# Kernel optimization log

Measured on AMD Instinct MI355X. Metric: run time of the kernel, lower is better.

The kernel has to match this reference:

```python
import jax, jax.numpy as jnp
import numpy as np

B, T, N, DIN = 32, 12, 512, 1
H, K, ED, HOR, OD = 64, 3, 10, 12, 1


def setup_inputs() -> dict:
    key = jax.random.key(0)
    ks = jax.random.split(key, 15)
    rn = lambda k, s, sc=0.1: jax.random.normal(k, s, jnp.float32) * sc
    return {
        "source": jax.random.normal(ks[0], (B, T, N, DIN), jnp.float32),
        "targets": jax.random.normal(ks[1], (B, HOR, N, OD), jnp.float32),
        # standard Gumbel(0,1) noise: -log(Exp(1)), matches torch's exponential_().log()
        "gumbel_noise": -jnp.log(jax.random.exponential(ks[2], (N, N, 2), jnp.float32)),
        "emb": jax.random.normal(ks[3], (N, ED), jnp.float32),
        "gw0": rn(ks[4], (ED, K, DIN + H, 2 * H)),
        "gb0": rn(ks[5], (ED, 2 * H)),
        "uw0": rn(ks[6], (ED, K, DIN + H, H)),
        "ub0": rn(ks[7], (ED, H)),
        "gw1": rn(ks[8], (ED, K, 2 * H, 2 * H)),
        "gb1": rn(ks[9], (ED, 2 * H)),
        "uw1": rn(ks[10], (ED, K, 2 * H, H)),
        "ub1": rn(ks[11], (ED, H)),
        "cw": rn(ks[12], (HOR * OD, 1, 1, H)),  # Conv2d(1, HOR*OD, (1, H)) weight
        "cb": rn(ks[13], (HOR * OD,)),
    }


def scaled_laplacian(emb, gnoise):
    sim = emb @ emb.T                                   # [N,N]
    nrm = jnp.linalg.norm(emb, axis=1, keepdims=True)
    lg = sim / (nrm @ nrm.T)
    lg = (lg + 1.0) / 2.0
    logits = jnp.stack([lg, 1.0 - lg], axis=-1)         # [N,N,2]
    # faithful to the pasted gumbel_softmax: y_soft = gumbels (no softmax), tau=1, hard=True
    y_soft = logits + gnoise
    idx = jnp.argmax(y_soft, axis=-1)
    y_hard = jax.nn.one_hot(idx, 2, dtype=logits.dtype)
    ret = y_hard - jax.lax.stop_gradient(y_soft) + y_soft
    adj = ret[:, :, 0] * (1.0 - jnp.eye(N, dtype=logits.dtype))  # zero diagonal
    d = jnp.sum(adj, axis=1)
    L = -adj + jnp.diag(d)                              # diag(adj)=0, so L diag = d
    lam = jnp.max(L) - jnp.min(L)
    tilde = 2.0 * L / lam - jnp.eye(N, dtype=logits.dtype)
    return tilde


def cheb_supports(tilde):
    sup = [jnp.eye(N, dtype=tilde.dtype), tilde]
    for _ in range(2, K):
        sup.append(2.0 * tilde @ sup[-1] - sup[-2])
    return jnp.stack(sup, axis=0)                       # [K,N,N]


def gconv(x, emb, supports, wp, bp):
    # x: [B,N,C]; wp: [ED,K,C,O]; bp: [ED,O]
    xg = jnp.einsum('knm,bmc->bnkc', supports, x)
    w = jnp.einsum('nd,dkio->nkio', emb, wp)
    b = emb @ bp                                        # [N,O]
    return jnp.einsum('bnki,nkio->bno', xg, w) + b


def run_layer(inputs, emb, supports, gw, gb, uw, ub):
    # inputs: [B,T,N,C] -> hidden states [B,T,N,H]
    h0 = jnp.zeros((inputs.shape[0], N, H), inputs.dtype)

    def step(h, x_t):
        xs = jnp.concatenate([x_t, h], axis=-1)
        zr = jax.nn.sigmoid(gconv(xs, emb, supports, gw, gb))
        z, r = zr[..., :H], zr[..., H:]
        cand = jnp.concatenate([x_t, z * h], axis=-1)
        hc = jnp.tanh(gconv(cand, emb, supports, uw, ub))
        h_new = r * h + (1.0 - r) * hc
        return h_new, h_new

    _, hs = jax.lax.scan(step, h0, jnp.swapaxes(inputs, 0, 1))
    return jnp.swapaxes(hs, 0, 1)


def reference(source, targets, gumbel_noise, emb, gw0, gb0, uw0, ub0,
              gw1, gb1, uw1, ub1, cw, cb):
    tilde = scaled_laplacian(emb, gumbel_noise)
    supports = cheb_supports(tilde)
    h1 = run_layer(source, emb, supports, gw0, gb0, uw0, ub0)
    h2 = run_layer(h1, emb, supports, gw1, gb1, uw1, ub1)
    last = h2[:, -1, :, :]                              # [B,N,H]
    # Conv2d(1, HOR*OD, (1,H)) over [B,1,N,H] == per-node linear
    y = jnp.einsum('bnh,oh->bon', last, cw[:, 0, 0, :]) + cb[None, :, None]
    y = y.reshape(-1, HOR, OD, N)
    return jnp.transpose(y, (0, 1, 3, 2))               # [B,HOR,N,OD]
```

## Files before the change

kernel.cpp:

```cpp
#include <hip/hip_runtime.h>
#include <math.h>

#define N_    512
#define B_    32
#define T_    12
#define H_    64
#define ED_   10
#define HOR_  12
#define OUTS_ 4096

typedef unsigned short ushort_t;
typedef __attribute__((ext_vector_type(4))) float f32x4;
typedef __attribute__((ext_vector_type(8))) __bf16 bf16x8;
typedef __attribute__((ext_vector_type(8))) short short8;

__device__ __forceinline__ float sigmoidf_(float x){ return 1.f/(1.f+expf(-x)); }
__device__ __forceinline__ float b2f(ushort_t u){ return __uint_as_float(((unsigned)u)<<16); }
__device__ __forceinline__ ushort_t f2b(float f){
  unsigned x = __float_as_uint(f);
  unsigned r = x + 0x7FFFu + ((x>>16)&1u);
  return (ushort_t)(r>>16);
}
__device__ __forceinline__ void stage16(const void* g, void* l){
  __builtin_amdgcn_global_load_lds(
    (const __attribute__((address_space(1))) unsigned int*)g,
    (__attribute__((address_space(3))) unsigned int*)l, 16, 0, 0);
}

__global__ __launch_bounds__(512) void k_norm(const float* __restrict__ emb, float* __restrict__ nrm){
  int n = threadIdx.x;
  if (n < N_){
    float s = 0.f;
    #pragma unroll
    for (int d=0; d<ED_; ++d){ float v = emb[n*ED_+d]; s += v*v; }
    nrm[n] = sqrtf(s);
  }
}

__global__ __launch_bounds__(256) void k_adj(const float* __restrict__ emb, const float* __restrict__ nrm,
                      const float* __restrict__ gn, ushort_t* __restrict__ Abf, float* __restrict__ dvec){
  __shared__ float ei[ED_];
  __shared__ float red[256];
  int i = blockIdx.x;
  if (threadIdx.x < ED_) ei[threadIdx.x] = emb[i*ED_+threadIdx.x];
  __syncthreads();
  float ni = nrm[i];
  float part = 0.f;
  for (int j = threadIdx.x; j < N_; j += 256){
    float dot = 0.f;
    #pragma unroll
    for (int d=0; d<ED_; ++d) dot += ei[d]*emb[j*ED_+d];
    float lg = (dot/(ni*nrm[j]) + 1.f)*0.5f;
    size_t gi = ((size_t)i*N_ + j)*2;
    float y0 = lg + gn[gi];
    float y1 = (1.f - lg) + gn[gi+1];
    bool a = (j != i && y0 >= y1);
    Abf[(size_t)i*N_ + j] = a ? (ushort_t)0x3F80 : (ushort_t)0;
    part += a ? 1.f : 0.f;
  }
  red[threadIdx.x] = part;
  __syncthreads();
  for (int s=128; s>0; s>>=1){
    if (threadIdx.x < s) red[threadIdx.x] += red[threadIdx.x+s];
    __syncthreads();
  }
  if (threadIdx.x==0) dvec[i] = red[0];
}

__global__ __launch_bounds__(512) void k_lam(const float* __restrict__ dvec, float* __restrict__ lam){
  __shared__ float red[512];
  red[threadIdx.x] = dvec[threadIdx.x];
  __syncthreads();
  for (int s=256; s>0; s>>=1){
    if (threadIdx.x < s) red[threadIdx.x] = fmaxf(red[threadIdx.x], red[threadIdx.x+s]);
    __syncthreads();
  }
  if (threadIdx.x==0){
    float maxd = red[0];
    lam[0] = maxd + (maxd > 0.f ? 1.f : 0.f);
  }
}

__global__ __launch_bounds__(256) void k_a2(const ushort_t* __restrict__ Abf, ushort_t* __restrict__ A2bf){
  __shared__ float ar[N_];
  int n = blockIdx.x;
  for (int p = threadIdx.x; p < N_; p += 256) ar[p] = b2f(Abf[(size_t)n*N_ + p]);
  __syncthreads();
  int m0 = threadIdx.x, m1 = threadIdx.x + 256;
  float a0 = 0.f, a1 = 0.f;
  for (int p=0; p<N_; ++p){
    float ap = ar[p];
    a0 += ap * b2f(Abf[(size_t)p*N_ + m0]);
    a1 += ap * b2f(Abf[(size_t)p*N_ + m1]);
  }
  A2bf[(size_t)n*N_ + m0] = f2b(a0);
  A2bf[(size_t)n*N_ + m1] = f2b(a1);
}

__global__ __launch_bounds__(256) void k_admats(const ushort_t* __restrict__ Abf, const float* __restrict__ dvec,
                        const float* __restrict__ lam, ushort_t* __restrict__ ADh){
  int idx = blockIdx.x*256 + threadIdx.x;
  int m = idx & (N_-1);
  float dm = 2.f*dvec[m]/lam[0] - 1.f;
  ADh[idx] = Abf[idx] ? f2b(dm) : (ushort_t)0;
}

#define XTILE_USH 8192
__global__ __launch_bounds__(256) void k_apply(
    const ushort_t* __restrict__ XH, const ushort_t* __restrict__ XL,
    const ushort_t* __restrict__ Abf, const ushort_t* __restrict__ A2bf, const ushort_t* __restrict__ ADh,
    float* __restrict__ P, float* __restrict__ Rm, float* __restrict__ Qm)
{
  __shared__ ushort_t lds[2*XTILE_USH + 4096];
  const int z = blockIdx.z;
  const ushort_t* M = (z==0)? Abf : (z==1)? A2bf : ADh;
  float* OUT = (z==0)? P : (z==1)? Rm : Qm;
  const int cBase = blockIdx.x<<7, nBase = blockIdx.y<<6;
  const int tid = threadIdx.x, lane = tid&63, w = tid>>6;
  const int lrow = lane>>3, lslot = lane&7;
  const int srck = lslot ^ (lrow&7);
  const char* g0 = (const char*)XH;
  const char* g1 = (const char*)XL;
  const char* g2 = (const char*)M;
  f32x4 acc[2][4];
  #pragma unroll
  for (int i=0;i<2;++i)
    #pragma unroll
    for (int j=0;j<4;++j) acc[i][j] = f32x4{0.f,0.f,0.f,0.f};
  const int fl = lane&15, kq = lane>>4;

  for (int kk=0; kk<512; kk+=64){
    #pragma unroll
    for (int s=0; s<10; ++s){
      int instId = w + s*4;
      int tile = instId>>4, inst = instId&15;
      const char* g = (tile==0? g0 : (tile==1? g1 : g2));
      int rb = (tile<2? cBase : nBase) + inst*8 + lrow;
      stage16(g + (size_t)rb*(N_*2) + kk*2 + srck*16,
              (char*)lds + tile*16384 + inst*1024);
    }
    __syncthreads();
    #pragma unroll
    for (int kh=0; kh<2; ++kh){
      bf16x8 ah[2], alo[2], bm[4];
      #pragma unroll
      for (int fi=0; fi<2; ++fi){
        int row = (w<<5) + (fi<<4) + fl;
        int off = (row<<6) + (((kq + (kh<<2)) ^ (row&7))<<3);
        ah[fi]  = *(const bf16x8*)&lds[off];
        alo[fi] = *(const bf16x8*)&lds[XTILE_USH + off];
      }
      #pragma unroll
      for (int fj=0; fj<4; ++fj){
        int row = (fj<<4) + fl;
        int off = (row<<6) + (((kq + (kh<<2)) ^ (row&7))<<3);
        bm[fj] = *(const bf16x8*)&lds[2*XTILE_USH + off];
      }
      #pragma unroll
      for (int fi=0; fi<2; ++fi)
        #pragma unroll
        for (int fj=0; fj<4; ++fj){
          acc[fi][fj] = __builtin_amdgcn_mfma_f32_16x16x32_bf16(ah[fi],  bm[fj], acc[fi][fj], 0,0,0);
          acc[fi][fj] = __builtin_amdgcn_mfma_f32_16x16x32_bf16(alo[fi], bm[fj], acc[fi][fj], 0,0,0);
        }
    }
    __syncthreads();
  }
  #pragma unroll
  for (int fi=0; fi<2; ++fi){
    int cg = cBase + (w<<5) + (fi<<4) + (kq<<2);
    #pragma unroll
    for (int fj=0; fj<4; ++fj){
      int ng = nBase + (fj<<4) + fl;
      float4 v = make_float4(acc[fi][fj][0], acc[fi][fj][1], acc[fi][fj][2], acc[fi][fj][3]);
      *(float4*)&OUT[(size_t)ng*OUTS_ + cg] = v;
    }
  }
}

__global__ __launch_bounds__(256) void k_wmax(const float* __restrict__ wp, const float* __restrict__ emb,
                       unsigned int* __restrict__ sb, int KI, int O, int KB){
  __shared__ float es[N_*ED_];
  __shared__ float sm[256];
  for (int e = threadIdx.x; e < N_*ED_; e += 256) es[e] = emb[e];
  __syncthreads();
  int G = 256/O;
  int o = threadIdx.x % O;
  int g = threadIdx.x / O;
  int KIend = min(KI, (int)(blockIdx.x+1)*KB);
  int n0 = blockIdx.y*128;
  size_t KIO = (size_t)KI*O;
  float m = 0.f;
  for (int ki = blockIdx.x*KB + g; ki < KIend; ki += G){
    float wv[ED_];
    #pragma unroll
    for (int d=0; d<ED_; ++d) wv[d] = wp[(size_t)d*KIO + (size_t)ki*O + o];
    for (int n=n0; n<n0+128; ++n){
      float a = 0.f;
      #pragma unroll
      for (int d=0; d<ED_; ++d) a += es[n*ED_+d]*wv[d];
      m = fmaxf(m, fabsf(a));
    }
  }
  sm[threadIdx.x] = m;
  __syncthreads();
  for (int s=128; s>=O; s>>=1){
    if (threadIdx.x < s) sm[threadIdx.x] = fmaxf(sm[threadIdx.x], sm[threadIdx.x+s]);
    __syncthreads();
  }
  if (threadIdx.x < O) atomicMax(&sb[o], __float_as_uint(sm[threadIdx.x]));
}

__global__ __launch_bounds__(256) void k_wquant(const float* __restrict__ wp, const float* __restrict__ emb,
                         const unsigned int* __restrict__ sb, short* __restrict__ W,
                         int KI, int O, int RS){
  __shared__ float es[N_*ED_];
  for (int e = threadIdx.x; e < N_*ED_; e += 256) es[e] = emb[e];
  __syncthreads();
  int KC = RS/8;
  int e = blockIdx.x*256 + threadIdx.x;
  if (e >= KC*O) return;
  int o = e % O, kc = e / O;
  int KIO = KI*O;
  float M = __uint_as_float(sb[o]);
  float inv = (M > 0.f) ? 32767.f/M : 0.f;
  float wv[8][ED_];
  #pragma unroll
  for (int km=0; km<8; ++km){
    int ki = kc*8 + km;
    #pragma unroll
    for (int d=0; d<ED_; ++d)
      wv[km][d] = (ki < KI) ? wp[(size_t)d*KIO + (size_t)ki*O + o] : 0.f;
  }
  int n0 = blockIdx.y*32;
  for (int n=n0; n<n0+32; ++n){
    short8 q;
    #pragma unroll
    for (int km=0; km<8; ++km){
      float a = 0.f;
      #pragma unroll
      for (int d=0; d<ED_; ++d) a += es[n*ED_+d]*wv[km][d];
      q[km] = (short)__float2int_rn(a*inv);
    }
    *(short8*)&W[(((size_t)n*KC + kc)*O + o)*8] = q;
  }
}

__global__ __launch_bounds__(256) void k_bias(const float* __restrict__ bp, const float* __restrict__ emb,
                       float* __restrict__ Bo, int O){
  int idx = blockIdx.x*256 + threadIdx.x;
  int o = idx % O, n = idx / O;
  float a = 0.f;
  #pragma unroll
  for (int d=0; d<ED_; ++d) a += emb[n*ED_+d]*bp[d*O+o];
  Bo[idx] = a;
}

__global__ void k_fill0(float* __restrict__ p, size_t n){
  size_t i = (size_t)blockIdx.x*blockDim.x + threadIdx.x;
  size_t stride = (size_t)gridDim.x*blockDim.x;
  for (; i<n; i+=stride) p[i] = 0.f;
}

__global__ __launch_bounds__(256) void k_btr(const float* __restrict__ S0, const float* __restrict__ S1,
        ushort_t* __restrict__ XH, ushort_t* __restrict__ XL, int CIN, int coff0, int coff1,
        const float* __restrict__ src, int t, int doSrc){
  __shared__ float Tt[64][65];
  const float* S = blockIdx.z ? S1 : S0;
  int coff = blockIdx.z ? coff1 : coff0;
  int mt = blockIdx.x, b = blockIdx.y;
  int r = threadIdx.x >> 6;
  int j = threadIdx.x & 63;
  #pragma unroll
  for (int rr=0; rr<16; ++rr){
    int m = mt*64 + rr*4 + r;
    Tt[rr*4+r][j] = S[((size_t)m*B_ + b)*H_ + j];
  }
  if (doSrc && blockIdx.z==0 && threadIdx.x < 64){
    int m = mt*64 + threadIdx.x;
    float x = src[((size_t)(b*T_+t))*N_ + m];
    size_t o = ((size_t)(b*CIN))*N_ + m;
    ushort_t xh = f2b(x);
    XH[o] = xh; XL[o] = f2b(x - b2f(xh));
  }
  __syncthreads();
  int mr = threadIdx.x & 63;
  int jq = threadIdx.x >> 6;
  #pragma unroll
  for (int jj=0; jj<16; ++jj){
    int jcol = jj*4 + jq;
    float x = Tt[mr][jcol];
    size_t idx = ((size_t)(b*CIN + coff + jcol))*N_ + mt*64 + mr;
    ushort_t xh = f2b(x);
    XH[idx] = xh;
    XL[idx] = f2b(x - b2f(xh));
  }
}

template<int KC, int NBJ, int OSTR, int AS>
__device__ __forceinline__ void contract_i16(const short* __restrict__ Wb,
                                             const float* __restrict__ A0,
                                             float acc[4][NBJ]){
  short8 w0,w1,w2,w3, p0,p1,p2,p3, q0,q1,q2,q3;
  {
    const short8* wp8 = (const short8*)(Wb);
    w0=wp8[0]; w1=wp8[1]; w2=wp8[2]; w3=wp8[3];
    const short8* pp8 = (const short8*)(Wb + OSTR);
    p0=pp8[0]; p1=pp8[1]; p2=pp8[2]; p3=pp8[3];
    q0=p0; q1=p1; q2=p2; q3=p3;
  }
  for (int kc=0; kc<KC; ++kc){
    if (kc+2 < KC){
      const short8* np8 = (const short8*)(Wb + (size_t)(kc+2)*OSTR);
      q0=np8[0]; q1=np8[1]; q2=np8[2]; q3=np8[3];
    }
    #pragma unroll
    for (int kh=0; kh<2; ++kh){
      f32x4 av[NBJ];
      #pragma unroll
      for (int bj=0; bj<NBJ; ++bj) av[bj] = *(const f32x4*)&A0[bj*AS + kc*8 + kh*4];
      #pragma unroll
      for (int u=0; u<4; ++u){
        float f0=(float)w0[kh*4+u], f1=(float)w1[kh*4+u];
        float f2v=(float)w2[kh*4+u], f3=(float)w3[kh*4+u];
        #pragma unroll
        for (int bj=0; bj<NBJ; ++bj){
          acc[0][bj] += av[bj][u]*f0;
          acc[1][bj] += av[bj][u]*f1;
          acc[2][bj] += av[bj][u]*f2v;
          acc[3][bj] += av[bj][u]*f3;
        }
      }
    }
    w0=p0; w1=p1; w2=p2; w3=p3;
    p0=q0; p1=q1; p2=q2; p3=q3;
  }
}

template<int CIN>
__global__ __launch_bounds__(256) void k_gate(
    const float* __restrict__ src, int t,
    const float* __restrict__ hx, const float* __restrict__ hy,
    const float* __restrict__ P, const float* __restrict__ Rm, const float* __restrict__ Qm,
    const float* __restrict__ dvec, const float* __restrict__ lam,
    const short* __restrict__ W, const float* __restrict__ Wsc, const float* __restrict__ Bb,
    const float* __restrict__ hstate,
    float* __restrict__ cand, float* __restrict__ rbuf)
{
  constexpr int O  = 128;
  constexpr int RS = (3*CIN + 7) & ~7;
  constexpr int KC = RS/8;
  constexpr int AS = RS + 4;
  __shared__ float A[B_*AS];
  int n = blockIdx.x;
  float lm = lam[0];
  float al = -2.f/lm;
  float dn = 2.f*dvec[n]/lm - 1.f;
  float c_r = 2.f*al*al, c_q = 2.f*al, c_p = 2.f*al*dn, c_x = 2.f*dn*dn - 1.f;
  for (int e = threadIdx.x; e < B_*CIN; e += 256){
    int b = e/CIN, c = e%CIN;
    float x;
    if (CIN==65) x = (c==0) ? src[((size_t)(b*T_+t))*N_ + n] : hx[(size_t)n*(B_*H_) + b*H_ + (c-1)];
    else         x = (c<H_) ? hx[(size_t)n*(B_*H_) + b*H_ + c] : hy[(size_t)n*(B_*H_) + b*H_ + (c-H_)];
    size_t pi = (size_t)n*OUTS_ + e;
    float pe = P[pi], re = Rm[pi], qe = Qm[pi];
    float* Ab = A + b*AS;
    Ab[c]         = x;
    Ab[CIN+c]     = al*pe + dn*x;
    Ab[2*CIN+c]   = c_r*re + c_q*qe + c_p*pe + c_x*x;
  }
  for (int e = threadIdx.x; e < B_*(AS-3*CIN); e += 256){
    int b = e/(AS-3*CIN), c = e%(AS-3*CIN);
    A[b*AS + 3*CIN + c] = 0.f;
  }
  __syncthreads();
  int ow = threadIdx.x & 31;
  int bq = threadIdx.x >> 5;
  int o0 = ow*4;
  float acc[4][4] = {};
  const short* Wb = W + ((size_t)n*KC*O + o0)*8;
  const float* A0 = A + (bq*4)*AS;
  contract_i16<KC,4,O*8,AS>(Wb, A0, acc);
  #pragma unroll
  for (int oj=0; oj<4; ++oj){
    int o = o0 + oj;
    float sc = Wsc[o]*(1.f/32767.f);
    float bias = Bb[n*O+o];
    if (o < H_){
      #pragma unroll
      for (int bj=0; bj<4; ++bj){
        int b = bq*4 + bj;
        float z = sigmoidf_(acc[oj][bj]*sc + bias);
        size_t hi = (size_t)n*(B_*H_) + b*H_ + o;
        cand[hi] = z*hstate[hi];
      }
    } else {
      int oo = o - H_;
      #pragma unroll
      for (int bj=0; bj<4; ++bj){
        int b = bq*4 + bj;
        rbuf[(size_t)n*(B_*H_) + b*H_ + oo] = sigmoidf_(acc[oj][bj]*sc + bias);
      }
    }
  }
}

template<int CIN>
__global__ __launch_bounds__(256) void k_update(
    const float* __restrict__ src, int t,
    const float* __restrict__ hx, const float* __restrict__ cand,
    const float* __restrict__ P, const float* __restrict__ Rm, const float* __restrict__ Qm,
    const float* __restrict__ dvec, const float* __restrict__ lam,
    const short* __restrict__ W, const float* __restrict__ Wsc, const float* __restrict__ Bb,
    const float* __restrict__ rbuf, float* __restrict__ h)
{
  constexpr int O  = 64;
  constexpr int RS = (3*CIN + 7) & ~7;
  constexpr int KC = RS/8;
  constexpr int AS = RS + 4;
  __shared__ float A[B_*AS];
  int n = blockIdx.x;
  float lm = lam[0];
  float al = -2.f/lm;
  float dn = 2.f*dvec[n]/lm - 1.f;
  float c_r = 2.f*al*al, c_q = 2.f*al, c_p = 2.f*al*dn, c_x = 2.f*dn*dn - 1.f;
  for (int e = threadIdx.x; e < B_*CIN; e += 256){
    int b = e/CIN, c = e%CIN;
    float x;
    if (CIN==65) x = (c==0) ? src[((size_t)(b*T_+t))*N_ + n] : cand[(size_t)n*(B_*H_) + b*H_ + (c-1)];
    else         x = (c<H_) ? hx[(size_t)n*(B_*H_) + b*H_ + c] : cand[(size_t)n*(B_*H_) + b*H_ + (c-H_)];
    size_t pi = (size_t)n*OUTS_ + e;
    float pe = P[pi], re = Rm[pi], qe = Qm[pi];
    float* Ab = A + b*AS;
    Ab[c]         = x;
    Ab[CIN+c]     = al*pe + dn*x;
    Ab[2*CIN+c]   = c_r*re + c_q*qe + c_p*pe + c_x*x;
  }
  for (int e = threadIdx.x; e < B_*(AS-3*CIN); e += 256){
    int b = e/(AS-3*CIN), c = e%(AS-3*CIN);
    A[b*AS + 3*CIN + c] = 0.f;
  }
  __syncthreads();
  int ow = threadIdx.x & 15;
  int bq = threadIdx.x >> 4;
  int o0 = ow*4;
  float acc[4][2] = {};
  const short* Wb = W + ((size_t)n*KC*O + o0)*8;
  const float* A0 = A + (bq*2)*AS;
  contract_i16<KC,2,O*8,AS>(Wb, A0, acc);
  #pragma unroll
  for (int oj=0; oj<4; ++oj){
    int o = o0 + oj;
    float sc = Wsc[o]*(1.f/32767.f);
    float bias = Bb[n*O+o];
    #pragma unroll
    for (int bj=0; bj<2; ++bj){
      int b = bq*2 + bj;
      float hc = tanhf(acc[oj][bj]*sc + bias);
      size_t hidx = (size_t)n*(B_*H_) + b*H_ + o;
      float r = rbuf[hidx];
      h[hidx] = r*h[hidx] + (1.f-r)*hc;
    }
  }
}

__global__ __launch_bounds__(256) void k_readout(const float* __restrict__ hB, const float* __restrict__ cw,
                          const float* __restrict__ cb, float* __restrict__ out){
  int idx = blockIdx.x*256 + threadIdx.x;
  int n = idx & (N_-1);
  int bo = idx >> 9;
  int o = bo % HOR_, b = bo / HOR_;
  float a = cb[o];
  #pragma unroll
  for (int j=0;j<H_;++j) a += hB[(size_t)n*(B_*H_) + b*H_ + j]*cw[o*H_+j];
  out[idx] = a;
}

extern "C" void kernel_launch(void* const* d_in, const int* in_sizes, int n_in,
                              void* d_out, int out_size, void* d_ws, size_t ws_size,
                              hipStream_t stream){
  (void)in_sizes; (void)n_in; (void)out_size; (void)ws_size;
  const float* src  = (const float*)d_in[0];
  const float* gn   = (const float*)d_in[2];
  const float* emb  = (const float*)d_in[3];
  const float* gw0  = (const float*)d_in[4];
  const float* gb0  = (const float*)d_in[5];
  const float* uw0  = (const float*)d_in[6];
  const float* ub0  = (const float*)d_in[7];
  const float* gw1  = (const float*)d_in[8];
  const float* gb1  = (const float*)d_in[9];
  const float* uw1  = (const float*)d_in[10];
  const float* ub1  = (const float*)d_in[11];
  const float* cw   = (const float*)d_in[12];
  const float* cb   = (const float*)d_in[13];
  float* out = (float*)d_out;

  const int RS0 = 200;
  const int RS1 = 384;

  char* ws = (char*)d_ws;
  size_t off = 0;
  auto alloc = [&](size_t bytes)->char*{
    char* p = ws + off; off = (off + bytes + 255) & ~(size_t)255; return p;
  };
  short* Wg0 = (short*)alloc((size_t)N_*128*RS0*2);
  short* Wu0 = (short*)alloc((size_t)N_*64*RS0*2);
  short* Wg1 = (short*)alloc((size_t)N_*128*RS1*2);
  short* Wu1 = (short*)alloc((size_t)N_*64*RS1*2);
  unsigned int* Sg0 = (unsigned int*)alloc(128*4);
  unsigned int* Su0 = (unsigned int*)alloc(64*4);
  unsigned int* Sg1 = (unsigned int*)alloc(128*4);
  unsigned int* Su1 = (unsigned int*)alloc(64*4);
  float* Bg0 = (float*)alloc((size_t)N_*128*4);
  float* Bu0 = (float*)alloc((size_t)N_*64*4);
  float* Bg1 = (float*)alloc((size_t)N_*128*4);
  float* Bu1 = (float*)alloc((size_t)N_*64*4);
  ushort_t* Abf  = (ushort_t*)alloc((size_t)N_*N_*2);
  ushort_t* A2bf = (ushort_t*)alloc((size_t)N_*N_*2);
  ushort_t* ADh  = (ushort_t*)alloc((size_t)N_*N_*2);
  float* dvec = (float*)alloc(N_*4);
  float* lam  = (float*)alloc(256);
  float* nrm  = (float*)alloc(N_*4);
  float* hA   = (float*)alloc((size_t)N_*B_*H_*4);
  float* hB   = (float*)alloc((size_t)N_*B_*H_*4);
  float* rbuf = (float*)alloc((size_t)N_*B_*H_*4);
  float* cand = (float*)alloc((size_t)N_*B_*H_*4);
  ushort_t* XH = (ushort_t*)alloc((size_t)4096*N_*2);
  ushort_t* XL = (ushort_t*)alloc((size_t)4096*N_*2);
  float* P  = (float*)alloc((size_t)N_*OUTS_*4);
  float* R  = (float*)alloc((size_t)N_*OUTS_*4);
  float* Q  = (float*)alloc((size_t)N_*OUTS_*4);

  const float* fSg0 = (const float*)Sg0;
  const float* fSu0 = (const float*)Su0;
  const float* fSg1 = (const float*)Sg1;
  const float* fSu1 = (const float*)Su1;

  k_norm<<<1,512,0,stream>>>(emb, nrm);
  k_adj<<<N_,256,0,stream>>>(emb, nrm, gn, Abf, dvec);
  k_lam<<<1,512,0,stream>>>(dvec, lam);
  k_a2<<<N_,256,0,stream>>>(Abf, A2bf);
  k_admats<<<(N_*N_)/256,256,0,stream>>>(Abf, dvec, lam, ADh);

  k_fill0<<<1,256,0,stream>>>((float*)Sg0, 384);
  k_wmax<<<dim3(17,4),256,0,stream>>>(gw0, emb, Sg0, 195, 128, 12);
  k_wmax<<<dim3(13,4),256,0,stream>>>(uw0, emb, Su0, 195, 64, 16);
  k_wmax<<<dim3(32,4),256,0,stream>>>(gw1, emb, Sg1, 384, 128, 12);
  k_wmax<<<dim3(24,4),256,0,stream>>>(uw1, emb, Su1, 384, 64, 16);
  k_wquant<<<dim3((25*128+255)/256,16),256,0,stream>>>(gw0, emb, Sg0, Wg0, 195, 128, RS0);
  k_wquant<<<dim3((25*64+255)/256,16),256,0,stream>>>(uw0, emb, Su0, Wu0, 195, 64, RS0);
  k_wquant<<<dim3((48*128)/256,16),256,0,stream>>>(gw1, emb, Sg1, Wg1, 384, 128, RS1);
  k_wquant<<<dim3((48*64)/256,16),256,0,stream>>>(uw1, emb, Su1, Wu1, 384, 64, RS1);
  k_bias<<<(N_*128)/256,256,0,stream>>>(gb0, emb, Bg0, 128);
  k_bias<<<(N_*64)/256,256,0,stream>>>(ub0, emb, Bu0, 64);
  k_bias<<<(N_*128)/256,256,0,stream>>>(gb1, emb, Bg1, 128);
  k_bias<<<(N_*64)/256,256,0,stream>>>(ub1, emb, Bu1, 64);

  k_fill0<<<2048,256,0,stream>>>(hA, (size_t)N_*B_*H_);
  k_fill0<<<2048,256,0,stream>>>(hB, (size_t)N_*B_*H_);

  for (int t=0; t<T_; ++t){
    k_btr<<<dim3(8,32,1),256,0,stream>>>(hA, hA, XH, XL, 65, 1, 1, src, t, 1);
    k_apply<<<dim3(17,8,3),256,0,stream>>>(XH, XL, Abf, A2bf, ADh, P, R, Q);
    k_gate<65><<<N_,256,0,stream>>>(src, t, hA, hA, P, R, Q, dvec, lam,
                                    Wg0, fSg0, Bg0, hA, cand, rbuf);
    k_btr<<<dim3(8,32,1),256,0,stream>>>(cand, cand, XH, XL, 65, 1, 1, nullptr, 0, 0);
    k_apply<<<dim3(17,8,3),256,0,stream>>>(XH, XL, Abf, A2bf, ADh, P, R, Q);
    k_update<65><<<N_,256,0,stream>>>(src, t, hA, cand, P, R, Q, dvec, lam,
                                      Wu0, fSu0, Bu0, rbuf, hA);
    k_btr<<<dim3(8,32,2),256,0,stream>>>(hA, hB, XH, XL, 128, 0, 64, nullptr, 0, 0);
    k_apply<<<dim3(32,8,3),256,0,stream>>>(XH, XL, Abf, A2bf, ADh, P, R, Q);
    k_gate<128><<<N_,256,0,stream>>>(nullptr, 0, hA, hB, P, R, Q, dvec, lam,
                                     Wg1, fSg1, Bg1, hB, cand, rbuf);
    k_btr<<<dim3(8,32,1),256,0,stream>>>(cand, cand, XH, XL, 128, 64, 64, nullptr, 0, 0);
    k_apply<<<dim3(32,8,3),256,0,stream>>>(XH, XL, Abf, A2bf, ADh, P, R, Q);
    k_update<128><<<N_,256,0,stream>>>(nullptr, 0, hA, cand, P, R, Q, dvec, lam,
                                       Wu1, fSu1, Bu1, rbuf, hB);
  }

  k_readout<<<(B_*HOR_*N_)/256,256,0,stream>>>(hB, cw, cb, out);
}
```

Before: 2.929 ms.

## Fuse three support-matrix GEMMs into one k_apply pass sharing the X tile

k_apply now computes the products against Abf, A2bf and ADh in a single block. It stages one 64-column X tile (hi and lo halves) plus all three 64-row matrix tiles, instead of launching a z=3 grid where each block reloads its own 128-column X tile. This cuts repeated X loads and doubles the number of x-blocks, at the cost of more accumulators per thread and smaller per-matrix tiles. Separately, the weight-scale max reduction drops float atomicMax in favour of per-block partial maxima in scratch plus a small reduction kernel.

```diff
diff --git a/kernel.cpp b/kernel.cpp
--- a/kernel.cpp
+++ b/kernel.cpp
@@ -105,26 +105,19 @@
   ADh[idx] = Abf[idx] ? f2b(dm) : (ushort_t)0;
 }
 
-#define XTILE_USH 8192
 __global__ __launch_bounds__(256) void k_apply(
     const ushort_t* __restrict__ XH, const ushort_t* __restrict__ XL,
     const ushort_t* __restrict__ Abf, const ushort_t* __restrict__ A2bf, const ushort_t* __restrict__ ADh,
     float* __restrict__ P, float* __restrict__ Rm, float* __restrict__ Qm)
 {
-  __shared__ ushort_t lds[2*XTILE_USH + 4096];
-  const int z = blockIdx.z;
-  const ushort_t* M = (z==0)? Abf : (z==1)? A2bf : ADh;
-  float* OUT = (z==0)? P : (z==1)? Rm : Qm;
-  const int cBase = blockIdx.x<<7, nBase = blockIdx.y<<6;
+  __shared__ ushort_t lds[5*4096];
+  const int cBase = blockIdx.x<<6, nBase = blockIdx.y<<6;
   const int tid = threadIdx.x, lane = tid&63, w = tid>>6;
   const int lrow = lane>>3, lslot = lane&7;
   const int srck = lslot ^ (lrow&7);
-  const char* g0 = (const char*)XH;
-  const char* g1 = (const char*)XL;
-  const char* g2 = (const char*)M;
-  f32x4 acc[2][4];
-  #pragma unroll
-  for (int i=0;i<2;++i)
+  f32x4 acc[3][4];
+  #pragma unroll
+  for (int i=0;i<3;++i)
     #pragma unroll
     for (int j=0;j<4;++j) acc[i][j] = f32x4{0.f,0.f,0.f,0.f};
   const int fl = lane&15, kq = lane>>4;
@@ -133,69 +126,66 @@
     #pragma unroll
     for (int s=0; s<10; ++s){
       int instId = w + s*4;
-      int tile = instId>>4, inst = instId&15;
-      const char* g = (tile==0? g0 : (tile==1? g1 : g2));
+      int tile = instId>>3;
+      int inst = instId&7;
+      const char* g = (tile==0)? (const char*)XH : (tile==1)? (const char*)XL :
+                      (tile==2)? (const char*)Abf : (tile==3)? (const char*)A2bf : (const char*)ADh;
       int rb = (tile<2? cBase : nBase) + inst*8 + lrow;
       stage16(g + (size_t)rb*(N_*2) + kk*2 + srck*16,
-              (char*)lds + tile*16384 + inst*1024);
+              (char*)lds + tile*8192 + inst*1024);
     }
     __syncthreads();
     #pragma unroll
     for (int kh=0; kh<2; ++kh){
-      bf16x8 ah[2], alo[2], bm[4];
-      #pragma unroll
-      for (int fi=0; fi<2; ++fi){
-        int row = (w<<5) + (fi<<4) + fl;
-        int off = (row<<6) + (((kq + (kh<<2)) ^ (row&7))<<3);
-        ah[fi]  = *(const bf16x8*)&lds[off];
-        alo[fi] = *(const bf16x8*)&lds[XTILE_USH + off];
+      int rowA = (w<<4) + fl;
+      int offA = (rowA<<6) + (((kq + (kh<<2)) ^ (rowA&7))<<3);
+      bf16x8 ah  = *(const bf16x8*)&lds[offA];
+      bf16x8 alo = *(const bf16x8*)&lds[4096 + offA];
+      bf16x8 bA[4], b2[4], bD[4];
+      #pragma unroll
+      for (int fj=0; fj<4; ++fj){
+        int rowB = (fj<<4) + fl;
+        int offB = (rowB<<6) + (((kq + (kh<<2)) ^ (rowB&7))<<3);
+        bA[fj] = *(const bf16x8*)&lds[2*4096 + offB];
+        b2[fj] = *(const bf16x8*)&lds[3*4096 + offB];
+        bD[fj] = *(const bf16x8*)&lds[4*4096 + offB];
       }
       #pragma unroll
       for (int fj=0; fj<4; ++fj){
-        int row = (fj<<4) + fl;
-        int off = (row<<6) + (((kq + (kh<<2)) ^ (row&7))<<3);
-        bm[fj] = *(const bf16x8*)&lds[2*XTILE_USH + off];
+        acc[0][fj] = __builtin_amdgcn_mfma_f32_16x16x32_bf16(ah,  bA[fj], acc[0][fj], 0,0,0);
+        acc[0][fj] = __builtin_amdgcn_mfma_f32_16x16x32_bf16(alo, bA[fj], acc[0][fj], 0,0,0);
+        acc[1][fj] = __builtin_amdgcn_mfma_f32_16x16x32_bf16(ah,  b2[fj], acc[1][fj], 0,0,0);
+        acc[1][fj] = __builtin_amdgcn_mfma_f32_16x16x32_bf16(alo, b2[fj], acc[1][fj], 0,0,0);
+        acc[2][fj] = __builtin_amdgcn_mfma_f32_16x16x32_bf16(ah,  bD[fj], acc[2][fj], 0,0,0);
+        acc[2][fj] = __builtin_amdgcn_mfma_f32_16x16x32_bf16(alo, bD[fj], acc[2][fj], 0,0,0);
       }
-      #pragma unroll
-      for (int fi=0; fi<2; ++fi)
-        #pragma unroll
-        for (int fj=0; fj<4; ++fj){
-          acc[fi][fj] = __builtin_amdgcn_mfma_f32_16x16x32_bf16(ah[fi],  bm[fj], acc[fi][fj], 0,0,0);
-          acc[fi][fj] = __builtin_amdgcn_mfma_f32_16x16x32_bf16(alo[fi], bm[fj], acc[fi][fj], 0,0,0);
-        }
     }
     __syncthreads();
   }
-  #pragma unroll
-  for (int fi=0; fi<2; ++fi){
-    int cg = cBase + (w<<5) + (fi<<4) + (kq<<2);
-    #pragma unroll
-    for (int fj=0; fj<4; ++fj){
-      int ng = nBase + (fj<<4) + fl;
-      float4 v = make_float4(acc[fi][fj][0], acc[fi][fj][1], acc[fi][fj][2], acc[fi][fj][3]);
-      *(float4*)&OUT[(size_t)ng*OUTS_ + cg] = v;
-    }
+  int cg = cBase + (w<<4) + (kq<<2);
+  #pragma unroll
+  for (int fj=0; fj<4; ++fj){
+    int ng = nBase + (fj<<4) + fl;
+    *(float4*)&P [(size_t)ng*OUTS_ + cg] = make_float4(acc[0][fj][0],acc[0][fj][1],acc[0][fj][2],acc[0][fj][3]);
+    *(float4*)&Rm[(size_t)ng*OUTS_ + cg] = make_float4(acc[1][fj][0],acc[1][fj][1],acc[1][fj][2],acc[1][fj][3]);
+    *(float4*)&Qm[(size_t)ng*OUTS_ + cg] = make_float4(acc[2][fj][0],acc[2][fj][1],acc[2][fj][2],acc[2][fj][3]);
   }
 }
 
 __global__ __launch_bounds__(256) void k_wmax(const float* __restrict__ wp, const float* __restrict__ emb,
-                       unsigned int* __restrict__ sb, int KI, int O, int KB){
+                       float* __restrict__ scratch, int KIO, int O){
   __shared__ float es[N_*ED_];
   __shared__ float sm[256];
   for (int e = threadIdx.x; e < N_*ED_; e += 256) es[e] = emb[e];
   __syncthreads();
-  int G = 256/O;
-  int o = threadIdx.x % O;
-  int g = threadIdx.x / O;
-  int KIend = min(KI, (int)(blockIdx.x+1)*KB);
-  int n0 = blockIdx.y*128;
-  size_t KIO = (size_t)KI*O;
+  int e = blockIdx.x*256 + threadIdx.x;
   float m = 0.f;
-  for (int ki = blockIdx.x*KB + g; ki < KIend; ki += G){
+  if (e < KIO){
     float wv[ED_];
     #pragma unroll
-    for (int d=0; d<ED_; ++d) wv[d] = wp[(size_t)d*KIO + (size_t)ki*O + o];
-    for (int n=n0; n<n0+128; ++n){
+    for (int d=0; d<ED_; ++d) wv[d] = wp[(size_t)d*KIO + e];
+    int n0 = blockIdx.y*256;
+    for (int n=n0; n<n0+256; ++n){
       float a = 0.f;
       #pragma unroll
       for (int d=0; d<ED_; ++d) a += es[n*ED_+d]*wv[d];
@@ -208,11 +198,21 @@
     if (threadIdx.x < s) sm[threadIdx.x] = fmaxf(sm[threadIdx.x], sm[threadIdx.x+s]);
     __syncthreads();
   }
-  if (threadIdx.x < O) atomicMax(&sb[o], __float_as_uint(sm[threadIdx.x]));
+  if (threadIdx.x < O)
+    scratch[(size_t)(blockIdx.x*gridDim.y + blockIdx.y)*O + threadIdx.x] = sm[threadIdx.x];
+}
+
+__global__ __launch_bounds__(128) void k_wred(const float* __restrict__ scratch,
+                       float* __restrict__ sb, int nb, int O){
+  int o = threadIdx.x;
+  if (o >= O) return;
+  float m = 0.f;
+  for (int b=0; b<nb; ++b) m = fmaxf(m, scratch[(size_t)b*O + o]);
+  sb[o] = m;
 }
 
 __global__ __launch_bounds__(256) void k_wquant(const float* __restrict__ wp, const float* __restrict__ emb,
-                         const unsigned int* __restrict__ sb, short* __restrict__ W,
+                         const float* __restrict__ sb, short* __restrict__ W,
                          int KI, int O, int RS){
   __shared__ float es[N_*ED_];
   for (int e = threadIdx.x; e < N_*ED_; e += 256) es[e] = emb[e];
@@ -222,7 +222,7 @@
   if (e >= KC*O) return;
   int o = e % O, kc = e / O;
   int KIO = KI*O;
-  float M = __uint_as_float(sb[o]);
+  float M = sb[o];
   float inv = (M > 0.f) ? 32767.f/M : 0.f;
   float wv[8][ED_];
   #pragma unroll
@@ -507,10 +507,11 @@
   short* Wu0 = (short*)alloc((size_t)N_*64*RS0*2);
   short* Wg1 = (short*)alloc((size_t)N_*128*RS1*2);
   short* Wu1 = (short*)alloc((size_t)N_*64*RS1*2);
-  unsigned int* Sg0 = (unsigned int*)alloc(128*4);
-  unsigned int* Su0 = (unsigned int*)alloc(64*4);
-  unsigned int* Sg1 = (unsigned int*)alloc(128*4);
-  unsigned int* Su1 = (unsigned int*)alloc(64*4);
+  float* Sg0 = (float*)alloc(128*4);
+  float* Su0 = (float*)alloc(64*4);
+  float* Sg1 = (float*)alloc(128*4);
+  float* Su1 = (float*)alloc(64*4);
+  float* wscr = (float*)alloc((size_t)512*128*4);
   float* Bg0 = (float*)alloc((size_t)N_*128*4);
   float* Bu0 = (float*)alloc((size_t)N_*64*4);
   float* Bg1 = (float*)alloc((size_t)N_*128*4);
@@ -531,22 +532,20 @@
   float* R  = (float*)alloc((size_t)N_*OUTS_*4);
   float* Q  = (float*)alloc((size_t)N_*OUTS_*4);
 
-  const float* fSg0 = (const float*)Sg0;
-  const float* fSu0 = (const float*)Su0;
-  const float* fSg1 = (const float*)Sg1;
-  const float* fSu1 = (const float*)Su1;
-
   k_norm<<<1,512,0,stream>>>(emb, nrm);
   k_adj<<<N_,256,0,stream>>>(emb, nrm, gn, Abf, dvec);
   k_lam<<<1,512,0,stream>>>(dvec, lam);
   k_a2<<<N_,256,0,stream>>>(Abf, A2bf);
   k_admats<<<(N_*N_)/256,256,0,stream>>>(Abf, dvec, lam, ADh);
 
-  k_fill0<<<1,256,0,stream>>>((float*)Sg0, 384);
-  k_wmax<<<dim3(17,4),256,0,stream>>>(gw0, emb, Sg0, 195, 128, 12);
-  k_wmax<<<dim3(13,4),256,0,stream>>>(uw0, emb, Su0, 195, 64, 16);
-  k_wmax<<<dim3(32,4),256,0,stream>>>(gw1, emb, Sg1, 384, 128, 12);
-  k_wmax<<<dim3(24,4),256,0,stream>>>(uw1, emb, Su1, 384, 64, 16);
+  k_wmax<<<dim3(98,2),256,0,stream>>>(gw0, emb, wscr, 195*128, 128);
+  k_wred<<<1,128,0,stream>>>(wscr, Sg0, 196, 128);
+  k_wmax<<<dim3(49,2),256,0,stream>>>(uw0, emb, wscr, 195*64, 64);
+  k_wred<<<1,128,0,stream>>>(wscr, Su0, 98, 64);
+  k_wmax<<<dim3(192,2),256,0,stream>>>(gw1, emb, wscr, 384*128, 128);
+  k_wred<<<1,128,0,stream>>>(wscr, Sg1, 384, 128);
+  k_wmax<<<dim3(96,2),256,0,stream>>>(uw1, emb, wscr, 384*64, 64);
+  k_wred<<<1,128,0,stream>>>(wscr, Su1, 192, 64);
   k_wquant<<<dim3((25*128+255)/256,16),256,0,stream>>>(gw0, emb, Sg0, Wg0, 195, 128, RS0);
   k_wquant<<<dim3((25*64+255)/256,16),256,0,stream>>>(uw0, emb, Su0, Wu0, 195, 64, RS0);
   k_wquant<<<dim3((48*128)/256,16),256,0,stream>>>(gw1, emb, Sg1, Wg1, 384, 128, RS1);
@@ -561,21 +560,21 @@
 
   for (int t=0; t<T_; ++t){
     k_btr<<<dim3(8,32,1),256,0,stream>>>(hA, hA, XH, XL, 65, 1, 1, src, t, 1);
-    k_apply<<<dim3(17,8,3),256,0,stream>>>(XH, XL, Abf, A2bf, ADh, P, R, Q);
+    k_apply<<<dim3(34,8),256,0,stream>>>(XH, XL, Abf, A2bf, ADh, P, R, Q);
     k_gate<65><<<N_,256,0,stream>>>(src, t, hA, hA, P, R, Q, dvec, lam,
-                                    Wg0, fSg0, Bg0, hA, cand, rbuf);
+                                    Wg0, Sg0, Bg0, hA, cand, rbuf);
     k_btr<<<dim3(8,32,1),256,0,stream>>>(cand, cand, XH, XL, 65, 1, 1, nullptr, 0, 0);
-    k_apply<<<dim3(17,8,3),256,0,stream>>>(XH, XL, Abf, A2bf, ADh, P, R, Q);
+    k_apply<<<dim3(34,8),256,0,stream>>>(XH, XL, Abf, A2bf, ADh, P, R, Q);
     k_update<65><<<N_,256,0,stream>>>(src, t, hA, cand, P, R, Q, dvec, lam,
-                                      Wu0, fSu0, Bu0, rbuf, hA);
+                                      Wu0, Su0, Bu0, rbuf, hA);
     k_btr<<<dim3(8,32,2),256,0,stream>>>(hA, hB, XH, XL, 128, 0, 64, nullptr, 0, 0);
-    k_apply<<<dim3(32,8,3),256,0,stream>>>(XH, XL, Abf, A2bf, ADh, P, R, Q);
+    k_apply<<<dim3(64,8),256,0,stream>>>(XH, XL, Abf, A2bf, ADh, P, R, Q);
     k_gate<128><<<N_,256,0,stream>>>(nullptr, 0, hA, hB, P, R, Q, dvec, lam,
-                                     Wg1, fSg1, Bg1, hB, cand, rbuf);
+                                     Wg1, Sg1, Bg1, hB, cand, rbuf);
     k_btr<<<dim3(8,32,1),256,0,stream>>>(cand, cand, XH, XL, 128, 64, 64, nullptr, 0, 0);
-    k_apply<<<dim3(32,8,3),256,0,stream>>>(XH, XL, Abf, A2bf, ADh, P, R, Q);
+    k_apply<<<dim3(64,8),256,0,stream>>>(XH, XL, Abf, A2bf, ADh, P, R, Q);
     k_update<128><<<N_,256,0,stream>>>(nullptr, 0, hA, cand, P, R, Q, dvec, lam,
-                                       Wu1, fSu1, Bu1, rbuf, hB);
+                                       Wu1, Su1, Bu1, rbuf, hB);
   }
 
   k_readout<<<(B_*HOR_*N_)/256,256,0,stream>>>(hB, cw, cb, out);
```

After: 2.888 ms. Within noise of the previous version (-1.4%).
